# Kernel optimization log

Measured on AMD Instinct MI355X. Metric: run time of the kernel, lower is better.

The kernel has to match this reference:

```python
import jax, jax.numpy as jnp
import numpy as np

N_EXPERTS = 24
TOP_K = 3
EGYPTIAN = (1.0 / 2.0, 1.0 / 3.0, 1.0 / 6.0)


def setup_inputs() -> dict:
    key = jax.random.key(0)
    ks = jax.random.split(key, 6)
    B, L, D, F = 4, 1024, 1024, 2048
    s_in = 1.0 / np.sqrt(D)
    s_ff = 1.0 / np.sqrt(F)
    return {
        "x": jax.random.normal(ks[0], (B, L, D), dtype=jnp.float32),
        "gate_w": jax.random.normal(ks[1], (N_EXPERTS, D), dtype=jnp.float32) * s_in,
        "w1": jax.random.normal(ks[2], (N_EXPERTS, D, F), dtype=jnp.float32) * s_in,
        "b1": jax.random.normal(ks[3], (N_EXPERTS, F), dtype=jnp.float32) * s_in,
        "w2": jax.random.normal(ks[4], (N_EXPERTS, F, D), dtype=jnp.float32) * s_ff,
        "b2": jax.random.normal(ks[5], (N_EXPERTS, D), dtype=jnp.float32) * s_ff,
    }


def reference(x, gate_w, w1, b1, w2, b2):
    B, L, D = x.shape
    xf = x.reshape(-1, D)                              # [T, D]
    logits = xf @ gate_w.T                             # [T, E]
    _, top_idx = jax.lax.top_k(logits, TOP_K)          # [T, K] (values unused by original math)
    eg = jnp.asarray(EGYPTIAN, dtype=x.dtype)          # fixed Egyptian combine weights
    # per-token, per-expert combine weight: sum_k eg[k] * [top_idx[t,k]==e]
    comb = jnp.einsum("tke,k->te", jax.nn.one_hot(top_idx, N_EXPERTS, dtype=x.dtype), eg)  # [T, E]
    out = jnp.zeros_like(xf)
    for e in range(N_EXPERTS):  # small fixed loop over experts
        h = jax.nn.relu(xf @ w1[e] + b1[e])            # [T, F]
        out = out + comb[:, e:e + 1] * (h @ w2[e] + b2[e])
    return out.reshape(B, L, D)
```

## Files before the change

kernel.cpp:

```cpp
#include <hip/hip_runtime.h>
#include <hip/hip_bf16.h>
#include <cstdint>
#include <cstddef>

#define E_EXPERTS 24
#define D_DIM 1024
#define F_DIM 2048

#define BM 128
#define BN 128
#define BK 64
#define LDK 72

typedef float f32x4 __attribute__((ext_vector_type(4)));
typedef short s16x8 __attribute__((ext_vector_type(8)));

static __device__ __forceinline__ unsigned short f2bf(float f) {
    union { float f; unsigned u; } v; v.f = f;
    unsigned r = v.u + 0x7FFFu + ((v.u >> 16) & 1u);
    return (unsigned short)(r >> 16);
}

__global__ __launch_bounds__(256) void k_gate(const float* __restrict__ x,
                                              const float* __restrict__ gw,
                                              int* __restrict__ top3, int T) {
    int wave = (blockIdx.x * 256 + threadIdx.x) >> 6;
    int lane = threadIdx.x & 63;
    if (wave >= T) return;
    const float* xr = x + (size_t)wave * D_DIM;
    f32x4 xv[4];
#pragma unroll
    for (int i = 0; i < 4; ++i) xv[i] = *(const f32x4*)(xr + i * 256 + lane * 4);
    float v0 = -1e30f, v1 = -1e30f, v2 = -1e30f;
    int i0 = 0, i1 = 0, i2 = 0;
    for (int e = 0; e < E_EXPERTS; ++e) {
        const float* gr = gw + (size_t)e * D_DIM;
        float d = 0.f;
#pragma unroll
        for (int i = 0; i < 4; ++i) {
            f32x4 g = *(const f32x4*)(gr + i * 256 + lane * 4);
            d += xv[i].x * g.x + xv[i].y * g.y + xv[i].z * g.z + xv[i].w * g.w;
        }
#pragma unroll
        for (int s = 32; s > 0; s >>= 1) d += __shfl_xor(d, s, 64);
        if (d > v0)      { v2 = v1; i2 = i1; v1 = v0; i1 = i0; v0 = d; i0 = e; }
        else if (d > v1) { v2 = v1; i2 = i1; v1 = d;  i1 = e; }
        else if (d > v2) { v2 = d;  i2 = e; }
    }
    if (lane == 0) {
        top3[wave * 3 + 0] = i0;
        top3[wave * 3 + 1] = i1;
        top3[wave * 3 + 2] = i2;
    }
}

__global__ __launch_bounds__(256) void k_count(const int* __restrict__ top3,
                                               int* __restrict__ offs,
                                               int* __restrict__ cnt, int T) {
    __shared__ int lc[E_EXPERTS];
    int t = threadIdx.x;
    if (t < E_EXPERTS) lc[t] = 0;
    __syncthreads();
    for (int i = t; i < T * 3; i += 256) atomicAdd(&lc[top3[i]], 1);
    __syncthreads();
    if (t == 0) {
        int acc = 0;
        for (int e = 0; e < E_EXPERTS; ++e) { offs[e] = acc; acc += lc[e]; }
        offs[E_EXPERTS] = acc;
    }
    if (t < E_EXPERTS) cnt[t] = 0;
}

__global__ __launch_bounds__(256) void k_fill(const int* __restrict__ top3,
                                              const int* __restrict__ offs,
                                              int* __restrict__ cnt,
                                              int* __restrict__ list,
                                              int* __restrict__ tslot, int T) {
    __shared__ int lc[E_EXPERTS], lbase[E_EXPERTS];
    int t = threadIdx.x;
    if (t < E_EXPERTS) lc[t] = 0;
    __syncthreads();
    int tok = blockIdx.x * 256 + t;
    int e[3], li[3];
    if (tok < T) {
#pragma unroll
        for (int k = 0; k < 3; ++k) {
            e[k] = top3[tok * 3 + k];
            li[k] = atomicAdd(&lc[e[k]], 1);
        }
    }
    __syncthreads();
    if (t < E_EXPERTS) lbase[t] = atomicAdd(&cnt[t], lc[t]);
    __syncthreads();
    if (tok < T) {
#pragma unroll
        for (int k = 0; k < 3; ++k) {
            int slot = offs[e[k]] + lbase[e[k]] + li[k];
            list[slot] = tok;
            tslot[tok * 3 + k] = slot;
        }
    }
}

__global__ __launch_bounds__(256) void k_gemm1(const float* __restrict__ x,
                                               const float* __restrict__ w1,
                                               const float* __restrict__ b1,
                                               const int* __restrict__ offs,
                                               const int* __restrict__ list,
                                               unsigned short* __restrict__ H) {
    const int e = blockIdx.z, mtile = blockIdx.y, ntile = blockIdx.x;
    const int offE = offs[e], cntE = offs[e + 1] - offE;
    if (mtile * BM >= cntE) return;
    __shared__ unsigned short Asl[BM][LDK];
    __shared__ unsigned short Bsl[BN][LDK];
    const int tid = threadIdx.x, lane = tid & 63, wid = tid >> 6;
    const int wm = wid >> 1, wn = wid & 1;
    const float* W = w1 + (size_t)e * D_DIM * F_DIM;

    const int ar = tid >> 1, ahalf = tid & 1;
    int arow = mtile * BM + ar;
    int tokA = (arow < cntE) ? list[offE + arow] : list[offE];
    const float* xr = x + (size_t)tokA * D_DIM;

    const int bn = tid & 127, bk = tid >> 7;
    const int ncol = ntile * BN + bn;

    f32x4 acc[4][4];
#pragma unroll
    for (int i = 0; i < 4; ++i)
#pragma unroll
        for (int j = 0; j < 4; ++j) acc[i][j] = (f32x4){0.f, 0.f, 0.f, 0.f};

    for (int kt = 0; kt < D_DIM / BK; ++kt) {
        const int kb = kt * BK;
#pragma unroll
        for (int j = 0; j < 4; ++j) {
            f32x4 a0 = *(const f32x4*)(xr + kb + ahalf * 32 + j * 8);
            f32x4 a1 = *(const f32x4*)(xr + kb + ahalf * 32 + j * 8 + 4);
            s16x8 p;
            p[0] = (short)f2bf(a0.x); p[1] = (short)f2bf(a0.y);
            p[2] = (short)f2bf(a0.z); p[3] = (short)f2bf(a0.w);
            p[4] = (short)f2bf(a1.x); p[5] = (short)f2bf(a1.y);
            p[6] = (short)f2bf(a1.z); p[7] = (short)f2bf(a1.w);
            *(s16x8*)&Asl[ar][ahalf * 32 + j * 8] = p;
        }
#pragma unroll
        for (int j8 = 0; j8 < 4; ++j8) {
            s16x8 p;
#pragma unroll
            for (int j = 0; j < 8; ++j) {
                float f = W[(size_t)(kb + bk * 32 + j8 * 8 + j) * F_DIM + ncol];
                p[j] = (short)f2bf(f);
            }
            *(s16x8*)&Bsl[bn][bk * 32 + j8 * 8] = p;
        }
        __syncthreads();
#pragma unroll
        for (int kk = 0; kk < 2; ++kk) {
            s16x8 fa[4], fb[4];
            const int k0 = kk * 32 + (lane >> 4) * 8;
#pragma unroll
            for (int mi = 0; mi < 4; ++mi)
                fa[mi] = *(const s16x8*)&Asl[wm * 64 + mi * 16 + (lane & 15)][k0];
#pragma unroll
            for (int ni = 0; ni < 4; ++ni)
                fb[ni] = *(const s16x8*)&Bsl[wn * 64 + ni * 16 + (lane & 15)][k0];
#pragma unroll
            for (int mi = 0; mi < 4; ++mi)
#pragma unroll
                for (int ni = 0; ni < 4; ++ni)
                    acc[mi][ni] = __builtin_amdgcn_mfma_f32_16x16x32_bf16(
                        fa[mi], fb[ni], acc[mi][ni], 0, 0, 0);
        }
        __syncthreads();
    }
    const float* bias = b1 + (size_t)e * F_DIM;
#pragma unroll
    for (int ni = 0; ni < 4; ++ni) {
        int c = ntile * BN + wn * 64 + ni * 16 + (lane & 15);
        float bv = bias[c];
#pragma unroll
        for (int mi = 0; mi < 4; ++mi) {
            int rl = wm * 64 + mi * 16 + ((lane >> 4) << 2);
#pragma unroll
            for (int i = 0; i < 4; ++i) {
                int rowe = mtile * BM + rl + i;
                if (rowe < cntE) {
                    float h = acc[mi][ni][i] + bv;
                    h = h > 0.f ? h : 0.f;
                    H[(size_t)(offE + rowe) * F_DIM + c] = f2bf(h);
                }
            }
        }
    }
}

__global__ __launch_bounds__(256) void k_gemm2(const unsigned short* __restrict__ H,
                                               const float* __restrict__ w2,
                                               const float* __restrict__ b2,
                                               const int* __restrict__ offs,
                                               float* __restrict__ Y) {
    const int e = blockIdx.z, mtile = blockIdx.y, ntile = blockIdx.x;
    const int offE = offs[e], cntE = offs[e + 1] - offE;
    if (mtile * BM >= cntE) return;
    __shared__ unsigned short Asl[BM][LDK];
    __shared__ unsigned short Bsl[BN][LDK];
    const int tid = threadIdx.x, lane = tid & 63, wid = tid >> 6;
    const int wm = wid >> 1, wn = wid & 1;
    const float* W = w2 + (size_t)e * F_DIM * D_DIM;

    const int ar = tid >> 1, ahalf = tid & 1;
    const unsigned short* hr = H + (size_t)(offE + mtile * BM + ar) * F_DIM;
    const int bn = tid & 127, bk = tid >> 7;
    const int ncol = ntile * BN + bn;

    f32x4 acc[4][4];
#pragma unroll
    for (int i = 0; i < 4; ++i)
#pragma unroll
        for (int j = 0; j < 4; ++j) acc[i][j] = (f32x4){0.f, 0.f, 0.f, 0.f};

    for (int kt = 0; kt < F_DIM / BK; ++kt) {
        const int kb = kt * BK;
#pragma unroll
        for (int j = 0; j < 4; ++j)
            *(s16x8*)&Asl[ar][ahalf * 32 + j * 8] =
                *(const s16x8*)(hr + kb + ahalf * 32 + j * 8);
#pragma unroll
        for (int j8 = 0; j8 < 4; ++j8) {
            s16x8 p;
#pragma unroll
            for (int j = 0; j < 8; ++j) {
                float f = W[(size_t)(kb + bk * 32 + j8 * 8 + j) * D_DIM + ncol];
                p[j] = (short)f2bf(f);
            }
            *(s16x8*)&Bsl[bn][bk * 32 + j8 * 8] = p;
        }
        __syncthreads();
#pragma unroll
        for (int kk = 0; kk < 2; ++kk) {
            s16x8 fa[4], fb[4];
            const int k0 = kk * 32 + (lane >> 4) * 8;
#pragma unroll
            for (int mi = 0; mi < 4; ++mi)
                fa[mi] = *(const s16x8*)&Asl[wm * 64 + mi * 16 + (lane & 15)][k0];
#pragma unroll
            for (int ni = 0; ni < 4; ++ni)
                fb[ni] = *(const s16x8*)&Bsl[wn * 64 + ni * 16 + (lane & 15)][k0];
#pragma unroll
            for (int mi = 0; mi < 4; ++mi)
#pragma unroll
                for (int ni = 0; ni < 4; ++ni)
                    acc[mi][ni] = __builtin_amdgcn_mfma_f32_16x16x32_bf16(
                        fa[mi], fb[ni], acc[mi][ni], 0, 0, 0);
        }
        __syncthreads();
    }
    const float* bias = b2 + (size_t)e * D_DIM;
#pragma unroll
    for (int ni = 0; ni < 4; ++ni) {
        int c = ntile * BN + wn * 64 + ni * 16 + (lane & 15);
        float bv = bias[c];
#pragma unroll
        for (int mi = 0; mi < 4; ++mi) {
            int rl = wm * 64 + mi * 16 + ((lane >> 4) << 2);
#pragma unroll
            for (int i = 0; i < 4; ++i) {
                int rowe = mtile * BM + rl + i;
                if (rowe < cntE)
                    Y[(size_t)(offE + rowe) * D_DIM + c] = acc[mi][ni][i] + bv;
            }
        }
    }
}

__global__ __launch_bounds__(256) void k_gather(const float* __restrict__ Y,
                                                const int* __restrict__ tslot,
                                                float* __restrict__ out, int T) {
    int idx = blockIdx.x * 256 + threadIdx.x;
    int t = idx >> 8, d4 = (idx & 255) * 4;
    if (t >= T) return;
    f32x4 y0 = *(const f32x4*)(Y + (size_t)tslot[t * 3 + 0] * D_DIM + d4);
    f32x4 y1 = *(const f32x4*)(Y + (size_t)tslot[t * 3 + 1] * D_DIM + d4);
    f32x4 y2 = *(const f32x4*)(Y + (size_t)tslot[t * 3 + 2] * D_DIM + d4);
    f32x4 o = y0 * 0.5f + y1 * (1.f / 3.f) + y2 * (1.f / 6.f);
    *(f32x4*)(out + (size_t)t * D_DIM + d4) = o;
}

extern "C" void kernel_launch(void* const* d_in, const int* in_sizes, int n_in,
                              void* d_out, int out_size, void* d_ws, size_t ws_size,
                              hipStream_t stream) {
    const float* x  = (const float*)d_in[0];
    const float* gw = (const float*)d_in[1];
    const float* w1 = (const float*)d_in[2];
    const float* b1 = (const float*)d_in[3];
    const float* w2 = (const float*)d_in[4];
    const float* b2 = (const float*)d_in[5];
    float* out = (float*)d_out;
    const int T = in_sizes[0] / D_DIM;

    char* ws = (char*)d_ws;
    int* offs  = (int*)ws;
    int* cnt   = (int*)(ws + 128);
    int* top3  = (int*)(ws + 256);
    int* tslot = (int*)(ws + 256 + (size_t)T * 3 * 4);
    int* list  = (int*)(ws + 256 + (size_t)T * 3 * 8);
    size_t hoff = (256 + (size_t)T * 3 * 12 + 4095) & ~(size_t)4095;
    unsigned short* H = (unsigned short*)(ws + hoff);
    size_t hbytes = ((size_t)T * 3 + BM) * F_DIM * 2;
    size_t yoff = (hoff + hbytes + 4095) & ~(size_t)4095;
    float* Y = (float*)(ws + yoff);

    const int mt = (T + BM - 1) / BM;

    k_gate<<<dim3((T * 64 + 255) / 256), 256, 0, stream>>>(x, gw, top3, T);
    k_count<<<1, 256, 0, stream>>>(top3, offs, cnt, T);
    k_fill<<<dim3((T + 255) / 256), 256, 0, stream>>>(top3, offs, cnt, list, tslot, T);
    k_gemm1<<<dim3(F_DIM / BN, mt, E_EXPERTS), 256, 0, stream>>>(x, w1, b1, offs, list, H);
    k_gemm2<<<dim3(D_DIM / BN, mt, E_EXPERTS), 256, 0, stream>>>(H, w2, b2, offs, Y);
    k_gather<<<dim3(T, 1, 1), 256, 0, stream>>>(Y, tslot, out, T);
}
```

Baseline: 751.2 us.

## Pre-transpose weights to bf16 and stage GEMM tiles via global_load_lds

Adds kernels that convert x to bf16 and transpose-convert each expert's w1/w2 into K-contiguous bf16 buffers every call. The GEMMs then load A and B tiles straight into LDS with 16-byte global_load_lds, replacing the strided per-element fp32 weight loads and in-loop conversions. The unpadded LDS layout may cause bank conflicts. Y is now stored as bf16, halving gather traffic at some precision cost. The per-call transposes add an extra full read and write of both weight tensors.

```diff
diff --git a/kernel.cpp b/kernel.cpp
--- a/kernel.cpp
+++ b/kernel.cpp
@@ -10,15 +10,55 @@
 #define BM 128
 #define BN 128
 #define BK 64
-#define LDK 72
 
 typedef float f32x4 __attribute__((ext_vector_type(4)));
 typedef short s16x8 __attribute__((ext_vector_type(8)));
+typedef unsigned short u16x4 __attribute__((ext_vector_type(4)));
 
 static __device__ __forceinline__ unsigned short f2bf(float f) {
     union { float f; unsigned u; } v; v.f = f;
     unsigned r = v.u + 0x7FFFu + ((v.u >> 16) & 1u);
     return (unsigned short)(r >> 16);
+}
+static __device__ __forceinline__ float bf2f(unsigned short h) {
+    union { unsigned u; float f; } v; v.u = (unsigned)h << 16;
+    return v.f;
+}
+
+#define GLL16(g, l) __builtin_amdgcn_global_load_lds(                         \
+    (const __attribute__((address_space(1))) unsigned int*)(g),               \
+    (__attribute__((address_space(3))) unsigned int*)(l), 16, 0, 0)
+
+__global__ __launch_bounds__(256) void k_cvt(const float* __restrict__ in,
+                                             unsigned short* __restrict__ out, int n) {
+    int i = (blockIdx.x * 256 + threadIdx.x) * 8;
+    if (i >= n) return;
+    f32x4 a = *(const f32x4*)(in + i);
+    f32x4 b = *(const f32x4*)(in + i + 4);
+    s16x8 p;
+    p[0] = (short)f2bf(a.x); p[1] = (short)f2bf(a.y);
+    p[2] = (short)f2bf(a.z); p[3] = (short)f2bf(a.w);
+    p[4] = (short)f2bf(b.x); p[5] = (short)f2bf(b.y);
+    p[6] = (short)f2bf(b.z); p[7] = (short)f2bf(b.w);
+    *(s16x8*)(out + i) = p;
+}
+
+__global__ __launch_bounds__(256) void k_tconv(const float* __restrict__ in,
+                                               unsigned short* __restrict__ out,
+                                               int R, int C) {
+    in  += (size_t)blockIdx.z * R * C;
+    out += (size_t)blockIdx.z * R * C;
+    __shared__ float tl[32][33];
+    const int rb = blockIdx.y * 32, cb = blockIdx.x * 32;
+    const int r = threadIdx.x >> 3, c4 = (threadIdx.x & 7) * 4;
+    f32x4 v = *(const f32x4*)(in + (size_t)(rb + r) * C + cb + c4);
+    tl[r][c4 + 0] = v.x; tl[r][c4 + 1] = v.y;
+    tl[r][c4 + 2] = v.z; tl[r][c4 + 3] = v.w;
+    __syncthreads();
+    u16x4 o;
+    o[0] = f2bf(tl[c4 + 0][r]); o[1] = f2bf(tl[c4 + 1][r]);
+    o[2] = f2bf(tl[c4 + 2][r]); o[3] = f2bf(tl[c4 + 3][r]);
+    *(u16x4*)(out + (size_t)(cb + r) * R + rb + c4) = o;
 }
 
 __global__ __launch_bounds__(256) void k_gate(const float* __restrict__ x,
@@ -102,8 +142,8 @@
     }
 }
 
-__global__ __launch_bounds__(256) void k_gemm1(const float* __restrict__ x,
-                                               const float* __restrict__ w1,
+__global__ __launch_bounds__(256) void k_gemm1(const unsigned short* __restrict__ xbf,
+                                               const unsigned short* __restrict__ w1t,
                                                const float* __restrict__ b1,
                                                const int* __restrict__ offs,
                                                const int* __restrict__ list,
@@ -111,19 +151,22 @@
     const int e = blockIdx.z, mtile = blockIdx.y, ntile = blockIdx.x;
     const int offE = offs[e], cntE = offs[e + 1] - offE;
     if (mtile * BM >= cntE) return;
-    __shared__ unsigned short Asl[BM][LDK];
-    __shared__ unsigned short Bsl[BN][LDK];
-    const int tid = threadIdx.x, lane = tid & 63, wid = tid >> 6;
-    const int wm = wid >> 1, wn = wid & 1;
-    const float* W = w1 + (size_t)e * D_DIM * F_DIM;
-
-    const int ar = tid >> 1, ahalf = tid & 1;
-    int arow = mtile * BM + ar;
-    int tokA = (arow < cntE) ? list[offE + arow] : list[offE];
-    const float* xr = x + (size_t)tokA * D_DIM;
-
-    const int bn = tid & 127, bk = tid >> 7;
-    const int ncol = ntile * BN + bn;
+    __shared__ unsigned short Asl[BM][BK];
+    __shared__ unsigned short Bsl[BN][BK];
+    const int tid = threadIdx.x, lane = tid & 63, w = tid >> 6;
+    const int wm = w >> 1, wn = w & 1;
+    const int l8 = lane >> 3, l7 = lane & 7;
+
+    size_t abase[4], bbase[4];
+#pragma unroll
+    for (int i = 0; i < 4; ++i) {
+        int r = w * 32 + i * 8 + l8;
+        int arow = mtile * BM + r;
+        int tok = (arow < cntE) ? list[offE + arow] : list[offE];
+        abase[i] = (size_t)tok * D_DIM + l7 * 8;
+        int n = ntile * BN + w * 32 + i * 8 + l8;
+        bbase[i] = ((size_t)e * F_DIM + n) * D_DIM + l7 * 8;
+    }
 
     f32x4 acc[4][4];
 #pragma unroll
@@ -134,26 +177,11 @@
     for (int kt = 0; kt < D_DIM / BK; ++kt) {
         const int kb = kt * BK;
 #pragma unroll
-        for (int j = 0; j < 4; ++j) {
-            f32x4 a0 = *(const f32x4*)(xr + kb + ahalf * 32 + j * 8);
-            f32x4 a1 = *(const f32x4*)(xr + kb + ahalf * 32 + j * 8 + 4);
-            s16x8 p;
-            p[0] = (short)f2bf(a0.x); p[1] = (short)f2bf(a0.y);
-            p[2] = (short)f2bf(a0.z); p[3] = (short)f2bf(a0.w);
-            p[4] = (short)f2bf(a1.x); p[5] = (short)f2bf(a1.y);
-            p[6] = (short)f2bf(a1.z); p[7] = (short)f2bf(a1.w);
-            *(s16x8*)&Asl[ar][ahalf * 32 + j * 8] = p;
-        }
-#pragma unroll
-        for (int j8 = 0; j8 < 4; ++j8) {
-            s16x8 p;
-#pragma unroll
-            for (int j = 0; j < 8; ++j) {
-                float f = W[(size_t)(kb + bk * 32 + j8 * 8 + j) * F_DIM + ncol];
-                p[j] = (short)f2bf(f);
-            }
-            *(s16x8*)&Bsl[bn][bk * 32 + j8 * 8] = p;
-        }
+        for (int i = 0; i < 4; ++i)
+            GLL16(xbf + abase[i] + kb, &Asl[w * 32 + i * 8][0]);
+#pragma unroll
+        for (int i = 0; i < 4; ++i)
+            GLL16(w1t + bbase[i] + kb, &Bsl[w * 32 + i * 8][0]);
         __syncthreads();
 #pragma unroll
         for (int kk = 0; kk < 2; ++kk) {
@@ -196,23 +224,27 @@
 }
 
 __global__ __launch_bounds__(256) void k_gemm2(const unsigned short* __restrict__ H,
-                                               const float* __restrict__ w2,
+                                               const unsigned short* __restrict__ w2t,
                                                const float* __restrict__ b2,
                                                const int* __restrict__ offs,
-                                               float* __restrict__ Y) {
+                                               unsigned short* __restrict__ Y) {
     const int e = blockIdx.z, mtile = blockIdx.y, ntile = blockIdx.x;
     const int offE = offs[e], cntE = offs[e + 1] - offE;
     if (mtile * BM >= cntE) return;
-    __shared__ unsigned short Asl[BM][LDK];
-    __shared__ unsigned short Bsl[BN][LDK];
-    const int tid = threadIdx.x, lane = tid & 63, wid = tid >> 6;
-    const int wm = wid >> 1, wn = wid & 1;
-    const float* W = w2 + (size_t)e * F_DIM * D_DIM;
-
-    const int ar = tid >> 1, ahalf = tid & 1;
-    const unsigned short* hr = H + (size_t)(offE + mtile * BM + ar) * F_DIM;
-    const int bn = tid & 127, bk = tid >> 7;
-    const int ncol = ntile * BN + bn;
+    __shared__ unsigned short Asl[BM][BK];
+    __shared__ unsigned short Bsl[BN][BK];
+    const int tid = threadIdx.x, lane = tid & 63, w = tid >> 6;
+    const int wm = w >> 1, wn = w & 1;
+    const int l8 = lane >> 3, l7 = lane & 7;
+
+    size_t abase[4], bbase[4];
+#pragma unroll
+    for (int i = 0; i < 4; ++i) {
+        int r = w * 32 + i * 8 + l8;
+        abase[i] = (size_t)(offE + mtile * BM + r) * F_DIM + l7 * 8;
+        int n = ntile * BN + w * 32 + i * 8 + l8;
+        bbase[i] = ((size_t)e * D_DIM + n) * F_DIM + l7 * 8;
+    }
 
     f32x4 acc[4][4];
 #pragma unroll
@@ -223,19 +255,11 @@
     for (int kt = 0; kt < F_DIM / BK; ++kt) {
         const int kb = kt * BK;
 #pragma unroll
-        for (int j = 0; j < 4; ++j)
-            *(s16x8*)&Asl[ar][ahalf * 32 + j * 8] =
-                *(const s16x8*)(hr + kb + ahalf * 32 + j * 8);
-#pragma unroll
-        for (int j8 = 0; j8 < 4; ++j8) {
-            s16x8 p;
-#pragma unroll
-            for (int j = 0; j < 8; ++j) {
-                float f = W[(size_t)(kb + bk * 32 + j8 * 8 + j) * D_DIM + ncol];
-                p[j] = (short)f2bf(f);
-            }
-            *(s16x8*)&Bsl[bn][bk * 32 + j8 * 8] = p;
-        }
+        for (int i = 0; i < 4; ++i)
+            GLL16(H + abase[i] + kb, &Asl[w * 32 + i * 8][0]);
+#pragma unroll
+        for (int i = 0; i < 4; ++i)
+            GLL16(w2t + bbase[i] + kb, &Bsl[w * 32 + i * 8][0]);
         __syncthreads();
 #pragma unroll
         for (int kk = 0; kk < 2; ++kk) {
@@ -268,22 +292,26 @@
             for (int i = 0; i < 4; ++i) {
                 int rowe = mtile * BM + rl + i;
                 if (rowe < cntE)
-                    Y[(size_t)(offE + rowe) * D_DIM + c] = acc[mi][ni][i] + bv;
+                    Y[(size_t)(offE + rowe) * D_DIM + c] = f2bf(acc[mi][ni][i] + bv);
             }
         }
     }
 }
 
-__global__ __launch_bounds__(256) void k_gather(const float* __restrict__ Y,
+__global__ __launch_bounds__(256) void k_gather(const unsigned short* __restrict__ Y,
                                                 const int* __restrict__ tslot,
                                                 float* __restrict__ out, int T) {
     int idx = blockIdx.x * 256 + threadIdx.x;
     int t = idx >> 8, d4 = (idx & 255) * 4;
     if (t >= T) return;
-    f32x4 y0 = *(const f32x4*)(Y + (size_t)tslot[t * 3 + 0] * D_DIM + d4);
-    f32x4 y1 = *(const f32x4*)(Y + (size_t)tslot[t * 3 + 1] * D_DIM + d4);
-    f32x4 y2 = *(const f32x4*)(Y + (size_t)tslot[t * 3 + 2] * D_DIM + d4);
-    f32x4 o = y0 * 0.5f + y1 * (1.f / 3.f) + y2 * (1.f / 6.f);
+    const unsigned short* y0 = Y + (size_t)tslot[t * 3 + 0] * D_DIM + d4;
+    const unsigned short* y1 = Y + (size_t)tslot[t * 3 + 1] * D_DIM + d4;
+    const unsigned short* y2 = Y + (size_t)tslot[t * 3 + 2] * D_DIM + d4;
+    u16x4 a = *(const u16x4*)y0, b = *(const u16x4*)y1, c = *(const u16x4*)y2;
+    f32x4 o;
+#pragma unroll
+    for (int j = 0; j < 4; ++j)
+        o[j] = bf2f(a[j]) * 0.5f + bf2f(b[j]) * (1.f / 3.f) + bf2f(c[j]) * (1.f / 6.f);
     *(f32x4*)(out + (size_t)t * D_DIM + d4) = o;
 }
 
@@ -305,18 +333,29 @@
     int* top3  = (int*)(ws + 256);
     int* tslot = (int*)(ws + 256 + (size_t)T * 3 * 4);
     int* list  = (int*)(ws + 256 + (size_t)T * 3 * 8);
-    size_t hoff = (256 + (size_t)T * 3 * 12 + 4095) & ~(size_t)4095;
-    unsigned short* H = (unsigned short*)(ws + hoff);
-    size_t hbytes = ((size_t)T * 3 + BM) * F_DIM * 2;
-    size_t yoff = (hoff + hbytes + 4095) & ~(size_t)4095;
-    float* Y = (float*)(ws + yoff);
+    size_t off = (256 + (size_t)T * 3 * 12 + 4095) & ~(size_t)4095;
+
+    unsigned short* xbf = (unsigned short*)(ws + off);
+    off += (size_t)T * D_DIM * 2;
+    unsigned short* H = (unsigned short*)(ws + off);
+    off += ((size_t)T * 3 + BM) * F_DIM * 2;
+    unsigned short* Y = (unsigned short*)(ws + off);
+    off += (size_t)T * 3 * D_DIM * 2;
+    off = (off + 4095) & ~(size_t)4095;
+    unsigned short* wt = (unsigned short*)(ws + off);
 
     const int mt = (T + BM - 1) / BM;
 
+    k_cvt<<<dim3((T * D_DIM) / (256 * 8)), 256, 0, stream>>>(x, xbf, T * D_DIM);
     k_gate<<<dim3((T * 64 + 255) / 256), 256, 0, stream>>>(x, gw, top3, T);
     k_count<<<1, 256, 0, stream>>>(top3, offs, cnt, T);
     k_fill<<<dim3((T + 255) / 256), 256, 0, stream>>>(top3, offs, cnt, list, tslot, T);
-    k_gemm1<<<dim3(F_DIM / BN, mt, E_EXPERTS), 256, 0, stream>>>(x, w1, b1, offs, list, H);
-    k_gemm2<<<dim3(D_DIM / BN, mt, E_EXPERTS), 256, 0, stream>>>(H, w2, b2, offs, Y);
+
+    k_tconv<<<dim3(F_DIM / 32, D_DIM / 32, E_EXPERTS), 256, 0, stream>>>(w1, wt, D_DIM, F_DIM);
+    k_gemm1<<<dim3(F_DIM / BN, mt, E_EXPERTS), 256, 0, stream>>>(xbf, wt, b1, offs, list, H);
+
+    k_tconv<<<dim3(D_DIM / 32, F_DIM / 32, E_EXPERTS), 256, 0, stream>>>(w2, wt, F_DIM, D_DIM);
+    k_gemm2<<<dim3(D_DIM / BN, mt, E_EXPERTS), 256, 0, stream>>>(H, wt, b2, offs, Y);
+
     k_gather<<<dim3(T, 1, 1), 256, 0, stream>>>(Y, tslot, out, T);
 }
```

New measurement: 784.0 us. 1.04x slower.
